# Kernel tuning notes

Hardware: AMD Instinct MI355X
Metric: run time of the kernel (lower is better)

The kernel has to match this reference:

```python
import jax, jax.numpy as jnp
import numpy as np

HEAD_NUM = 16
PAD = 0.0
MASKS_FUTURE = True


def setup_inputs() -> dict:
    key = jax.random.key(0)
    ks = jax.random.split(key, 7)
    B, S, D = 2, 2048, 1024
    scale = 0.02
    return {
        "q": jax.random.normal(ks[0], (B, S, D), dtype=jnp.float32),
        "k": jax.random.normal(ks[1], (B, S, D), dtype=jnp.float32),
        "v": jax.random.normal(ks[2], (B, S, D), dtype=jnp.float32),
        "w_q": jax.random.normal(ks[3], (D, D), dtype=jnp.float32) * scale,
        "w_k": jax.random.normal(ks[4], (D, D), dtype=jnp.float32) * scale,
        "w_v": jax.random.normal(ks[5], (D, D), dtype=jnp.float32) * scale,
        "w_o": jax.random.normal(ks[6], (D, D), dtype=jnp.float32) * scale,
    }


def _split_head(x):
    # [B, S, D] -> [B, H, S, D/H]
    B, S, D = x.shape
    return x.reshape(B, S, HEAD_NUM, D // HEAD_NUM).transpose(0, 2, 1, 3)


def reference(q, k, v, w_q, w_k, w_v, w_o):
    qp = _split_head(q @ w_q)  # [B, H, Sq, dk]
    kp = _split_head(k @ w_k)  # [B, H, Sk, dk]
    vp = _split_head(v @ w_v)  # [B, H, Sk, dv]
    d_k = qp.shape[-1]
    scores = jnp.einsum("bhqd,bhkd->bhqk", qp, kp) / jnp.sqrt(jnp.float32(d_k))
    # mask where scores equal PAD (faithful to tf.equal(head_qk, PAD))
    mask = scores == PAD
    if MASKS_FUTURE:
        # tf.linalg.band_part(mask, -1, 0): keep lower triangle, zero elsewhere
        Sq, Sk = scores.shape[-2], scores.shape[-1]
        tril = jnp.tril(jnp.ones((Sq, Sk), dtype=bool))
        mask = mask & tril
    neg = jnp.finfo(jnp.float32).min
    scores = jnp.where(mask, neg, scores)
    attn = jax.nn.softmax(scores, axis=-1)
    # keep_prob = 1.0 -> dropout is identity
    attn = jnp.where(mask, PAD, attn)
    out = jnp.einsum("bhqk,bhkd->bhqd", attn, vp)  # [B, H, Sq, dv/H]
    B, H, S, dh = out.shape
    concat = out.transpose(0, 2, 1, 3).reshape(B, S, H * dh)
    return concat @ w_o
```

## Files before the change

### kernel.cpp

```cpp
#include <hip/hip_runtime.h>
#include <hip/hip_bf16.h>

typedef unsigned short u16;
typedef unsigned int u32;
typedef short short8 __attribute__((ext_vector_type(8)));
typedef float float4v __attribute__((ext_vector_type(4)));
typedef u32 u32x2 __attribute__((ext_vector_type(2)));

#define SEQ 2048
#define DIM 1024
#define NHEAD 16
#define MROWS 4096
#define NE ((size_t)MROWS * DIM)
#define WN ((size_t)DIM * DIM)

#if __has_builtin(__builtin_amdgcn_exp2f)
#define EXP2(x) __builtin_amdgcn_exp2f(x)
#else
#define EXP2(x) exp2f(x)
#endif

__device__ inline u16 f2bf(float f) {
    union { float f; unsigned u; } v; v.f = f;
    unsigned r = v.u + 0x7fffu + ((v.u >> 16) & 1u);
    return (u16)(r >> 16);
}
__device__ inline float bf2f(u16 s) {
    union { unsigned u; float f; } v; v.u = ((unsigned)s) << 16;
    return v.f;
}
__device__ inline u32 pk2bf(float a, float b) {
    union { __hip_bfloat162 h; u32 u; } cv;
    cv.h = __float22bfloat162_rn(float2{a, b});
    return cv.u;
}
__device__ inline void gld16(const void* g, void* l) {
    __builtin_amdgcn_global_load_lds(
        (const __attribute__((address_space(1))) void*)g,
        (__attribute__((address_space(3))) void*)l, 16, 0, 0);
}

__global__ __launch_bounds__(256) void prep(
    const float* __restrict__ q, const float* __restrict__ k,
    const float* __restrict__ v, const float* __restrict__ w_q,
    const float* __restrict__ w_k, const float* __restrict__ w_v,
    const float* __restrict__ w_o, u16* __restrict__ Abf, u16* __restrict__ Wt)
{
    __shared__ u16 T[64 * 66];
    const int bx = blockIdx.x;
    const int tid = threadIdx.x;

    if (bx < 6144) {
        const int z = bx >> 11, xb = bx & 2047;
        const float* s = (z == 0) ? q : (z == 1) ? k : v;
        const size_t i = ((size_t)xb * 256 + tid) * 8;
        float4v a = *(const float4v*)(s + i);
        float4v b = *(const float4v*)(s + i + 4);
        short8 o;
        for (int e = 0; e < 4; e++) { o[e] = (short)f2bf(a[e]); o[4 + e] = (short)f2bf(b[e]); }
        *(short8*)(Abf + (size_t)z * NE + i) = o;
        return;
    }

    const int t = bx - 6144;
    const int z = t & 3, tile = t >> 2;
    const float* src = (z == 0) ? w_o : (z == 1) ? w_q : (z == 2) ? w_k : w_v;
    const int kt = (tile >> 4) * 64, nt = (tile & 15) * 64;
    {
        const int row = tid >> 2, cg = (tid & 3) * 16;
        const float* sp = src + (size_t)(kt + row) * DIM + nt + cg;
        for (int i4 = 0; i4 < 4; i4++) {
            float4v f = *(const float4v*)(sp + i4 * 4);
            for (int e = 0; e < 4; e++)
                T[row * 66 + cg + i4 * 4 + e] = f2bf(f[e]);
        }
    }
    __syncthreads();
    {
        const int nr = tid >> 2, kg = (tid & 3) * 16;
        u16* dp = Wt + (size_t)z * WN + (size_t)(nt + nr) * DIM + kt + kg;
        short8 o0, o1;
        for (int e = 0; e < 8; e++) {
            o0[e] = (short)T[(kg + e) * 66 + nr];
            o1[e] = (short)T[(kg + 8 + e) * 66 + nr];
        }
        *(short8*)(dp) = o0;
        *(short8*)(dp + 8) = o1;
    }
}

__global__ __launch_bounds__(256) void gemm_qkv(
    const u16* __restrict__ Abf, const u16* __restrict__ Wtg, u16* __restrict__ QKVb)
{
    __shared__ u16 SMEM[2 * 128 * 64];
    u16* Alds = SMEM;
    u16* Wlds = SMEM + 128 * 64;

    const int z = blockIdx.z;
    const u16* A = Abf + (size_t)z * NE;
    const u16* W = Wtg + (size_t)(z + 1) * WN;

    const int tid = threadIdx.x;
    const int lane = tid & 63, w = tid >> 6;
    const int quad = lane >> 4, l16 = lane & 15;
    const int wr = w >> 1, wc = w & 1;
    const int m0 = blockIdx.x * 128, n0 = blockIdx.y * 128;

    float4v acc[4][4];
    float4v vz = {0.f, 0.f, 0.f, 0.f};
    for (int i = 0; i < 4; i++)
        for (int j = 0; j < 4; j++) acc[i][j] = vz;

    for (int k0 = 0; k0 < DIM; k0 += 64) {
        for (int i = 0; i < 4; i++) {
            const int c = tid + i * 256;
            const int row = c >> 3, scc = (c & 7) ^ (row & 7);
            gld16(A + (size_t)(m0 + row) * DIM + k0 + scc * 8, &Alds[c * 8]);
            gld16(W + (size_t)(n0 + row) * DIM + k0 + scc * 8, &Wlds[c * 8]);
        }
        __syncthreads();

        for (int s = 0; s < 2; s++) {
            short8 a[4], b[4];
            for (int i = 0; i < 4; i++) {
                const int row = wr * 64 + i * 16 + l16;
                a[i] = *(const short8*)&Alds[row * 64 + (((s * 4 + quad) ^ (row & 7)) * 8)];
            }
            for (int j = 0; j < 4; j++) {
                const int row = wc * 64 + j * 16 + l16;
                b[j] = *(const short8*)&Wlds[row * 64 + (((s * 4 + quad) ^ (row & 7)) * 8)];
            }
            for (int i = 0; i < 4; i++)
                for (int j = 0; j < 4; j++)
                    acc[i][j] = __builtin_amdgcn_mfma_f32_16x16x32_bf16(a[i], b[j], acc[i][j], 0, 0, 0);
        }
        __syncthreads();
    }

    if (z < 2) {
        for (int i = 0; i < 4; i++) {
            int row = m0 + wr * 64 + i * 16 + quad * 4;
            for (int j = 0; j < 4; j++) {
                int col = n0 + wc * 64 + j * 16 + l16;
                for (int r = 0; r < 4; r++)
                    QKVb[(size_t)z * NE + (size_t)(row + r) * DIM + col] = f2bf(acc[i][j][r]);
            }
        }
        return;
    }

    u16* T = SMEM;
    for (int i = 0; i < 4; i++)
        for (int j = 0; j < 4; j++) {
            const int d = wc * 64 + j * 16 + l16;
            for (int r = 0; r < 4; r++) {
                const int s = wr * 64 + i * 16 + quad * 4 + r;
                T[d * 128 + (((s >> 3) ^ (d & 7)) * 8) + (s & 7)] = f2bf(acc[i][j][r]);
            }
        }
    __syncthreads();
    {
        u16* Vt = QKVb + 2 * NE;
        const int b = m0 >> 11, s_loc = m0 & 2047, h0 = n0 >> 6;
        const int c = lane & 15;
        for (int p = 0; p < 8; p++) {
            const int d = w * 32 + (lane >> 4) * 8 + p;
            short8 val = *(const short8*)&T[d * 128 + ((c ^ (d & 7)) * 8)];
            u16* dp = Vt + ((size_t)(b * 16 + h0 + (d >> 6)) * 64 + (d & 63)) * SEQ + s_loc + c * 8;
            *(short8*)dp = val;
        }
    }
}

__global__ __launch_bounds__(256) void gemm_out(
    const u16* __restrict__ Cb, const u16* __restrict__ Wtg, float* __restrict__ out)
{
    __shared__ u16 Alds[64 * 64];
    __shared__ u16 Wlds[128 * 64];
    const u16* W = Wtg;

    const int tid = threadIdx.x;
    const int lane = tid & 63, w = tid >> 6;
    const int quad = lane >> 4, l16 = lane & 15;
    const int wr = w >> 1, wc = w & 1;
    const int m0 = blockIdx.x * 64, n0 = blockIdx.y * 128;

    float4v acc[2][4];
    float4v vz = {0.f, 0.f, 0.f, 0.f};
    for (int i = 0; i < 2; i++)
        for (int j = 0; j < 4; j++) acc[i][j] = vz;

    for (int k0 = 0; k0 < DIM; k0 += 64) {
        {
            for (int i = 0; i < 2; i++) {
                const int c = tid + i * 256;
                const int row = c >> 3, scc = (c & 7) ^ (row & 7);
                gld16(Cb + (size_t)(m0 + row) * DIM + k0 + scc * 8, &Alds[c * 8]);
            }
            for (int i = 0; i < 4; i++) {
                const int c = tid + i * 256;
                const int row = c >> 3, scc = (c & 7) ^ (row & 7);
                gld16(W + (size_t)(n0 + row) * DIM + k0 + scc * 8, &Wlds[c * 8]);
            }
        }
        __syncthreads();

        for (int s = 0; s < 2; s++) {
            short8 a[2], b[4];
            for (int i = 0; i < 2; i++) {
                const int row = wr * 32 + i * 16 + l16;
                a[i] = *(const short8*)&Alds[row * 64 + (((s * 4 + quad) ^ (row & 7)) * 8)];
            }
            for (int j = 0; j < 4; j++) {
                const int row = wc * 64 + j * 16 + l16;
                b[j] = *(const short8*)&Wlds[row * 64 + (((s * 4 + quad) ^ (row & 7)) * 8)];
            }
            for (int i = 0; i < 2; i++)
                for (int j = 0; j < 4; j++)
                    acc[i][j] = __builtin_amdgcn_mfma_f32_16x16x32_bf16(a[i], b[j], acc[i][j], 0, 0, 0);
        }
        __syncthreads();
    }

    for (int i = 0; i < 2; i++) {
        int row = m0 + wr * 32 + i * 16 + quad * 4;
        for (int j = 0; j < 4; j++) {
            int col = n0 + wc * 64 + j * 16 + l16;
            for (int r = 0; r < 4; r++)
                out[(size_t)(row + r) * DIM + col] = acc[i][j][r];
        }
    }
}

__global__ __launch_bounds__(256) void attn_kernel(
    const u16* __restrict__ Q, const u16* __restrict__ K,
    const u16* __restrict__ Vtg, u16* __restrict__ O)
{
    __shared__ u16 Klds[128 * 64];
    __shared__ u16 Vt[64 * 128];
    __shared__ u16 Pl[4][64 * 40];
    __shared__ float Llds[4][64];
    float* bufA = (float*)Klds;
    float* bufB = (float*)Vt;

    const int bh = blockIdx.x;
    const int q0 = blockIdx.y * 64;
    const int tid = threadIdx.x;
    const int lane = tid & 63, w = tid >> 6;
    const int quad = lane >> 4, l16 = lane & 15;

    const size_t base = (size_t)(bh >> 4) * SEQ * DIM + (bh & 15) * 64;
    const u16* Qp = Q + base;
    const u16* Kp = K + base;
    u16* Op = O + base;
    const u16* Vp = Vtg + (size_t)bh * 64 * SEQ;

    short8 qb[4][2];
    {
        const float sc = 0.125f * 1.44269504088896f;
        for (int qc = 0; qc < 4; qc++)
            for (int s = 0; s < 2; s++) {
                short8 t = *(const short8*)(Qp + (size_t)(q0 + qc * 16 + l16) * DIM + s * 32 + quad * 8);
                for (int e = 0; e < 8; e++) t[e] = (short)f2bf(bf2f((u16)t[e]) * sc);
                qb[qc][s] = t;
            }
    }

    float4v acc[4][4];
    float4v vz = {0.f, 0.f, 0.f, 0.f};
    for (int qc = 0; qc < 4; qc++)
        for (int nb = 0; nb < 4; nb++) acc[qc][nb] = vz;
    float lp[4] = {0.f, 0.f, 0.f, 0.f};

    u16* pw = Pl[w];

    for (int kt = 0; kt < SEQ / 128; kt++) {
        const int k0 = kt * 128;
        for (int i = 0; i < 4; i++) {
            const int ck = tid + i * 256;
            const int rk = ck >> 3, sk = (ck & 7) ^ (rk & 7);
            gld16(Kp + (size_t)(k0 + rk) * DIM + sk * 8, &Klds[ck * 8]);
            const int cv = tid + i * 256;
            const int dv = cv >> 4, pv = cv & 15;
            const int sv = (pv & 8) | ((pv ^ (dv & 7)) & 7);
            gld16(Vp + (size_t)dv * SEQ + k0 + sv * 8, &Vt[cv * 8]);
        }
        __syncthreads();

        float4v st[2][4];
        for (int kr = 0; kr < 2; kr++) {
            const int row = w * 32 + kr * 16 + l16;
            short8 ka0 = *(const short8*)&Klds[row * 64 + ((quad ^ (l16 & 7)) * 8)];
            short8 ka1 = *(const short8*)&Klds[row * 64 + (((4 + quad) ^ (l16 & 7)) * 8)];
            for (int qc = 0; qc < 4; qc++) {
                float4v t = __builtin_amdgcn_mfma_f32_16x16x32_bf16(ka0, qb[qc][0], vz, 0, 0, 0);
                st[kr][qc] = __builtin_amdgcn_mfma_f32_16x16x32_bf16(ka1, qb[qc][1], t, 0, 0, 0);
            }
        }

        for (int kr = 0; kr < 2; kr++)
            for (int qc = 0; qc < 4; qc++) {
                float p0 = EXP2(st[kr][qc][0]), p1 = EXP2(st[kr][qc][1]);
                float p2 = EXP2(st[kr][qc][2]), p3 = EXP2(st[kr][qc][3]);
                lp[qc] += (p0 + p1) + (p2 + p3);
                u32x2 pk; pk[0] = pk2bf(p0, p1); pk[1] = pk2bf(p2, p3);
                *(u32x2*)((u32*)pw + (qc * 16 + l16) * 20 + kr * 8 + quad * 2) = pk;
            }
        asm volatile("" ::: "memory");

        short8 pa[4], vb[4];
        for (int qc = 0; qc < 4; qc++)
            pa[qc] = *(const short8*)&pw[(qc * 16 + l16) * 40 + quad * 8];
        for (int nb = 0; nb < 4; nb++) {
            const int gk = w * 4 + quad;
            const int pos = (gk & 8) | ((gk ^ (l16 & 7)) & 7);
            vb[nb] = *(const short8*)&Vt[(nb * 16 + l16) * 128 + pos * 8];
        }
        for (int qc = 0; qc < 4; qc++)
            for (int nb = 0; nb < 4; nb++)
                acc[qc][nb] = __builtin_amdgcn_mfma_f32_16x16x32_bf16(pa[qc], vb[nb], acc[qc][nb], 0, 0, 0);
        __syncthreads();
    }

    for (int qc = 0; qc < 4; qc++) {
        lp[qc] += __shfl_xor(lp[qc], 16);
        lp[qc] += __shfl_xor(lp[qc], 32);
    }
    if (quad == 0)
        for (int qc = 0; qc < 4; qc++) Llds[w][qc * 16 + l16] = lp[qc];

    if (w == 0 || w == 2) {
        float* buf = (w == 0) ? bufA : bufB;
        for (int qc = 0; qc < 4; qc++)
            for (int nb = 0; nb < 4; nb++)
                for (int r = 0; r < 4; r++)
                    buf[(qc * 16 + quad * 4 + r) * 64 + nb * 16 + l16] = acc[qc][nb][r];
    }
    __syncthreads();
    if (w == 1 || w == 3) {
        float* buf = (w == 1) ? bufA : bufB;
        for (int qc = 0; qc < 4; qc++)
            for (int nb = 0; nb < 4; nb++)
                for (int r = 0; r < 4; r++)
                    buf[(qc * 16 + quad * 4 + r) * 64 + nb * 16 + l16] += acc[qc][nb][r];
    }
    __syncthreads();

    {
        const int q = tid >> 2, dg = (tid & 3) * 16;
        const float l = Llds[0][q] + Llds[1][q] + Llds[2][q] + Llds[3][q];
        const float inv = 1.0f / l;
        short8 o0, o1;
        for (int e = 0; e < 8; e++) {
            o0[e] = (short)f2bf((bufA[q * 64 + dg + e] + bufB[q * 64 + dg + e]) * inv);
            o1[e] = (short)f2bf((bufA[q * 64 + dg + 8 + e] + bufB[q * 64 + dg + 8 + e]) * inv);
        }
        u16* dp = Op + (size_t)(q0 + q) * DIM + dg;
        *(short8*)(dp) = o0;
        *(short8*)(dp + 8) = o1;
    }
}

extern "C" void kernel_launch(void* const* d_in, const int* in_sizes, int n_in,
                              void* d_out, int out_size, void* d_ws, size_t ws_size,
                              hipStream_t stream)
{
    const float* q   = (const float*)d_in[0];
    const float* k   = (const float*)d_in[1];
    const float* v   = (const float*)d_in[2];
    const float* w_q = (const float*)d_in[3];
    const float* w_k = (const float*)d_in[4];
    const float* w_v = (const float*)d_in[5];
    const float* w_o = (const float*)d_in[6];
    float* out = (float*)d_out;

    u16* Abf  = (u16*)d_ws;
    u16* Wt   = Abf + 3 * NE;
    u16* QKVb = Wt + 4 * WN;
    u16* Cb   = Abf;

    dim3 blk(256);
    prep<<<dim3(7168), blk, 0, stream>>>(q, k, v, w_q, w_k, w_v, w_o, Abf, Wt);
    gemm_qkv<<<dim3(32, 8, 3), blk, 0, stream>>>(Abf, Wt, QKVb);
    attn_kernel<<<dim3(32, 32), blk, 0, stream>>>(QKVb, QKVb + NE, QKVb + 2 * NE, Cb);
    gemm_out<<<dim3(64, 8), blk, 0, stream>>>(Cb, Wt, out);
}
```

Baseline: 237.3 us.

## Fold Q scale into projection epilogue and alias P buffer onto K tile

Applies the softmax scale and log2e factor to Q when the QKV projection writes it, so the attention kernel loads Q fragments directly without the per-element bf16 rescale. The per-wave P staging buffer now reuses each wave's slice of the K LDS tile after K fragments are loaded into registers, which removes the separate 20KB Pl array, and launch bounds request 4 blocks per SM. The goal is lower LDS and register pressure for higher occupancy. The risks are register spills under the tighter bound and bank conflicts from the unpadded P row stride. Reusing K LDS is only safe because each wave reads its own K rows before overwriting them.

After: 342.1 us. +44.1%, slower.

```diff
diff --git a/kernel.cpp b/kernel.cpp
--- a/kernel.cpp
+++ b/kernel.cpp
@@ -138,12 +138,13 @@
     }
 
     if (z < 2) {
+        const float sc = (z == 0) ? 0.125f * 1.44269504088896f : 1.0f;
         for (int i = 0; i < 4; i++) {
             int row = m0 + wr * 64 + i * 16 + quad * 4;
             for (int j = 0; j < 4; j++) {
                 int col = n0 + wc * 64 + j * 16 + l16;
                 for (int r = 0; r < 4; r++)
-                    QKVb[(size_t)z * NE + (size_t)(row + r) * DIM + col] = f2bf(acc[i][j][r]);
+                    QKVb[(size_t)z * NE + (size_t)(row + r) * DIM + col] = f2bf(acc[i][j][r] * sc);
             }
         }
         return;
@@ -191,17 +192,15 @@
         for (int j = 0; j < 4; j++) acc[i][j] = vz;
 
     for (int k0 = 0; k0 < DIM; k0 += 64) {
-        {
-            for (int i = 0; i < 2; i++) {
-                const int c = tid + i * 256;
-                const int row = c >> 3, scc = (c & 7) ^ (row & 7);
-                gld16(Cb + (size_t)(m0 + row) * DIM + k0 + scc * 8, &Alds[c * 8]);
-            }
-            for (int i = 0; i < 4; i++) {
-                const int c = tid + i * 256;
-                const int row = c >> 3, scc = (c & 7) ^ (row & 7);
-                gld16(W + (size_t)(n0 + row) * DIM + k0 + scc * 8, &Wlds[c * 8]);
-            }
+        for (int i = 0; i < 2; i++) {
+            const int c = tid + i * 256;
+            const int row = c >> 3, scc = (c & 7) ^ (row & 7);
+            gld16(Cb + (size_t)(m0 + row) * DIM + k0 + scc * 8, &Alds[c * 8]);
+        }
+        for (int i = 0; i < 4; i++) {
+            const int c = tid + i * 256;
+            const int row = c >> 3, scc = (c & 7) ^ (row & 7);
+            gld16(W + (size_t)(n0 + row) * DIM + k0 + scc * 8, &Wlds[c * 8]);
         }
         __syncthreads();
 
@@ -232,13 +231,12 @@
     }
 }
 
-__global__ __launch_bounds__(256) void attn_kernel(
+__global__ __launch_bounds__(256, 4) void attn_kernel(
     const u16* __restrict__ Q, const u16* __restrict__ K,
     const u16* __restrict__ Vtg, u16* __restrict__ O)
 {
     __shared__ u16 Klds[128 * 64];
     __shared__ u16 Vt[64 * 128];
-    __shared__ u16 Pl[4][64 * 40];
     __shared__ float Llds[4][64];
     float* bufA = (float*)Klds;
     float* bufB = (float*)Vt;
@@ -256,15 +254,9 @@
     const u16* Vp = Vtg + (size_t)bh * 64 * SEQ;
 
     short8 qb[4][2];
-    {
-        const float sc = 0.125f * 1.44269504088896f;
-        for (int qc = 0; qc < 4; qc++)
-            for (int s = 0; s < 2; s++) {
-                short8 t = *(const short8*)(Qp + (size_t)(q0 + qc * 16 + l16) * DIM + s * 32 + quad * 8);
-                for (int e = 0; e < 8; e++) t[e] = (short)f2bf(bf2f((u16)t[e]) * sc);
-                qb[qc][s] = t;
-            }
-    }
+    for (int qc = 0; qc < 4; qc++)
+        for (int s = 0; s < 2; s++)
+            qb[qc][s] = *(const short8*)(Qp + (size_t)(q0 + qc * 16 + l16) * DIM + s * 32 + quad * 8);
 
     float4v acc[4][4];
     float4v vz = {0.f, 0.f, 0.f, 0.f};
@@ -272,7 +264,7 @@
         for (int nb = 0; nb < 4; nb++) acc[qc][nb] = vz;
     float lp[4] = {0.f, 0.f, 0.f, 0.f};
 
-    u16* pw = Pl[w];
+    u16* pw = Klds + w * 32 * 64;
 
     for (int kt = 0; kt < SEQ / 128; kt++) {
         const int k0 = kt * 128;
@@ -287,16 +279,19 @@
         }
         __syncthreads();
 
-        float4v st[2][4];
+        short8 ka[2][2];
         for (int kr = 0; kr < 2; kr++) {
             const int row = w * 32 + kr * 16 + l16;
-            short8 ka0 = *(const short8*)&Klds[row * 64 + ((quad ^ (l16 & 7)) * 8)];
-            short8 ka1 = *(const short8*)&Klds[row * 64 + (((4 + quad) ^ (l16 & 7)) * 8)];
+            ka[kr][0] = *(const short8*)&Klds[row * 64 + ((quad ^ (l16 & 7)) * 8)];
+            ka[kr][1] = *(const short8*)&Klds[row * 64 + (((4 + quad) ^ (l16 & 7)) * 8)];
+        }
+
+        float4v st[2][4];
+        for (int kr = 0; kr < 2; kr++)
             for (int qc = 0; qc < 4; qc++) {
-                float4v t = __builtin_amdgcn_mfma_f32_16x16x32_bf16(ka0, qb[qc][0], vz, 0, 0, 0);
-                st[kr][qc] = __builtin_amdgcn_mfma_f32_16x16x32_bf16(ka1, qb[qc][1], t, 0, 0, 0);
-            }
-        }
+                float4v t = __builtin_amdgcn_mfma_f32_16x16x32_bf16(ka[kr][0], qb[qc][0], vz, 0, 0, 0);
+                st[kr][qc] = __builtin_amdgcn_mfma_f32_16x16x32_bf16(ka[kr][1], qb[qc][1], t, 0, 0, 0);
+            }
 
         for (int kr = 0; kr < 2; kr++)
             for (int qc = 0; qc < 4; qc++) {
@@ -304,13 +299,13 @@
                 float p2 = EXP2(st[kr][qc][2]), p3 = EXP2(st[kr][qc][3]);
                 lp[qc] += (p0 + p1) + (p2 + p3);
                 u32x2 pk; pk[0] = pk2bf(p0, p1); pk[1] = pk2bf(p2, p3);
-                *(u32x2*)((u32*)pw + (qc * 16 + l16) * 20 + kr * 8 + quad * 2) = pk;
+                *(u32x2*)((u32*)pw + (qc * 16 + l16) * 16 + kr * 8 + quad * 2) = pk;
             }
         asm volatile("" ::: "memory");
 
         short8 pa[4], vb[4];
         for (int qc = 0; qc < 4; qc++)
-            pa[qc] = *(const short8*)&pw[(qc * 16 + l16) * 40 + quad * 8];
+            pa[qc] = *(const short8*)&pw[(qc * 16 + l16) * 32 + quad * 8];
         for (int nb = 0; nb < 4; nb++) {
             const int gk = w * 4 + quad;
             const int pos = (gk & 8) | ((gk ^ (l16 & 7)) & 7);
```
